# Performance work log

Hardware: AMD Instinct MI355X
Metric: run time of the kernel (lower is better)

## Reference

```python
import jax, jax.numpy as jnp
import numpy as np

D = 1024
H = 16
HD = D // H


def setup_inputs() -> dict:
    key = jax.random.key(0)
    ks = jax.random.split(key, 5)
    s = 1.0 / np.sqrt(D)
    return {
        "inputs": jax.random.normal(ks[0], (2, 2048, D), dtype=jnp.float32),
        "Wq": jax.random.normal(ks[1], (D, D), dtype=jnp.float32) * s,
        "bq": jnp.zeros((D,), jnp.float32),
        "Wk": jax.random.normal(ks[2], (D, D), dtype=jnp.float32) * s,
        "bk": jnp.zeros((D,), jnp.float32),
        "Wv": jax.random.normal(ks[3], (D, D), dtype=jnp.float32) * s,
        "bv": jnp.zeros((D,), jnp.float32),
        "Wo": jax.random.normal(ks[4], (D, D), dtype=jnp.float32) * s,
        "bo": jnp.zeros((D,), jnp.float32),
    }


def reference(inputs, Wq, bq, Wk, bk, Wv, bv, Wo, bo):
    B, S, _ = inputs.shape
    def split_heads(x):  # [B,S,D] -> [B,H,S,hd]
        return x.reshape(B, S, H, HD).transpose(0, 2, 1, 3)
    q = split_heads(inputs @ Wq + bq)
    k = split_heads(inputs @ Wk + bk)
    v = split_heads(inputs @ Wv + bv)
    scale = 1.0 / jnp.sqrt(jnp.asarray(HD, inputs.dtype))
    scores = jnp.einsum("bhsd,bhtd->bhst", q, k) * scale  # [B,H,S,S]
    weights = jax.nn.softmax(scores, axis=-1)
    attn = jnp.einsum("bhst,bhtd->bhsd", weights, v)
    concat = attn.transpose(0, 2, 1, 3).reshape(B, S, D)
    return concat @ Wo + bo
```

## Files before the change

kernel.cpp:

```cpp
#include <hip/hip_runtime.h>


typedef __bf16 bf16x8 __attribute__((ext_vector_type(8)));
typedef float  f32x4  __attribute__((ext_vector_type(4)));

#if __has_builtin(__builtin_amdgcn_exp2f)
#define EXPFN(x) __builtin_amdgcn_exp2f(x)
#define QSCALE (0.125f * 1.44269504088896f)
#else
#define EXPFN(x) __expf(x)
#define QSCALE 0.125f
#endif

#define LDKP 74

__device__ __forceinline__ unsigned short f2bf(float f) {
    unsigned int u = __float_as_uint(f);
    u += 0x7FFFu + ((u >> 16) & 1u);
    return (unsigned short)(u >> 16);
}

__device__ __forceinline__ void gload16(const void* g, void* l) {
    __builtin_amdgcn_global_load_lds(
        (const __attribute__((address_space(1))) void*)g,
        (__attribute__((address_space(3))) void*)l, 16, 0, 0);
}

#define WAIT0_BARRIER() asm volatile("s_waitcnt vmcnt(0)\n\ts_barrier" ::: "memory")

__global__ __launch_bounds__(256) void cast_x_kernel(
    const float4* __restrict__ X, ushort4* __restrict__ Xb, int n4) {
    int i = blockIdx.x * 256 + threadIdx.x;
    if (i < n4) {
        float4 v = X[i];
        ushort4 o;
        o.x = f2bf(v.x); o.y = f2bf(v.y); o.z = f2bf(v.z); o.w = f2bf(v.w);
        Xb[i] = o;
    }
}

__global__ __launch_bounds__(256) void transpose_w_kernel(
    const float* __restrict__ Wq, const float* __restrict__ Wk,
    const float* __restrict__ Wv, const float* __restrict__ Wo,
    unsigned short* __restrict__ Wt_all) {
    __shared__ float tile[32][33];
    const int z = blockIdx.z;
    const float* W = (z == 0) ? Wq : (z == 1) ? Wk : (z == 2) ? Wv : Wo;
    unsigned short* Wt = Wt_all + (size_t)z * 1024 * 1024;
    int c0 = blockIdx.x * 32, r0 = blockIdx.y * 32;
    int x = threadIdx.x, y = threadIdx.y;
    for (int j = 0; j < 32; j += 8)
        tile[y + j][x] = W[(r0 + y + j) * 1024 + c0 + x];
    __syncthreads();
    for (int j = 0; j < 32; j += 8)
        Wt[(c0 + y + j) * 1024 + r0 + x] = f2bf(tile[x][y + j]);
}

__global__ __launch_bounds__(256) void gemm_qkv_kernel(
    const unsigned short* __restrict__ Xb, const unsigned short* __restrict__ Wt_all,
    const float* __restrict__ bq, const float* __restrict__ bk,
    const float* __restrict__ bv,
    unsigned short* __restrict__ Qb, unsigned short* __restrict__ Kb,
    unsigned short* __restrict__ Vt) {
    const int z = blockIdx.z;
    const int x0 = blockIdx.x * 128;
    const int y0 = blockIdx.y * 128;

    const unsigned short* Ap;
    const unsigned short* Bp;
    if (z < 2) {
        Ap = Xb + (size_t)x0 * 1024;
        Bp = Wt_all + (size_t)z * 1024 * 1024 + (size_t)y0 * 1024;
    } else {
        Ap = Wt_all + (size_t)2 * 1024 * 1024 + (size_t)y0 * 1024;
        Bp = Xb + (size_t)x0 * 1024;
    }

    __shared__ __align__(16) unsigned short As[2][128 * 64];
    __shared__ __align__(16) unsigned short Bs[2][128 * 64];

    const int tid = threadIdx.x;
    const int lane = tid & 63, wave = tid >> 6;
    const int quad = lane >> 4, l15 = lane & 15;
    const int wrow = (wave >> 1) * 64, wcol = (wave & 1) * 64;

    f32x4 acc[4][4] = {};

    const int srow = lane >> 3;
    const int ch8  = (lane & 7) * 8;
    const int swz  = (((lane & 7) ^ srow)) * 8;
    const int sw   = (l15 & 7);

    #pragma unroll
    for (int c = 0; c < 4; c++) {
        int r = c * 32 + wave * 8 + srow;
        gload16(Ap + (size_t)r * 1024 + 0 + swz, &As[0][r * 64 + ch8]);
        gload16(Bp + (size_t)r * 1024 + 0 + swz, &Bs[0][r * 64 + ch8]);
    }

    for (int k = 0; k < 16; k++) {
        const int cur = k & 1, nxt = cur ^ 1;
        WAIT0_BARRIER();
        if (k < 15) {
            int k0 = (k + 1) * 64;
            #pragma unroll
            for (int c = 0; c < 4; c++) {
                int r = c * 32 + wave * 8 + srow;
                gload16(Ap + (size_t)r * 1024 + k0 + swz, &As[nxt][r * 64 + ch8]);
                gload16(Bp + (size_t)r * 1024 + k0 + swz, &Bs[nxt][r * 64 + ch8]);
            }
        }
        #pragma unroll
        for (int kk = 0; kk < 2; kk++) {
            bf16x8 af[4], bfr[4];
            #pragma unroll
            for (int i = 0; i < 4; i++)
                af[i] = *(const bf16x8*)&As[cur][(wrow + i * 16 + l15) * 64 +
                                                (((kk * 4 + quad) ^ sw)) * 8];
            #pragma unroll
            for (int j = 0; j < 4; j++)
                bfr[j] = *(const bf16x8*)&Bs[cur][(wcol + j * 16 + l15) * 64 +
                                                 (((kk * 4 + quad) ^ sw)) * 8];
            #pragma unroll
            for (int i = 0; i < 4; i++)
                #pragma unroll
                for (int j = 0; j < 4; j++)
                    acc[i][j] = __builtin_amdgcn_mfma_f32_16x16x32_bf16(
                        af[i], bfr[j], acc[i][j], 0, 0, 0);
        }
    }

    if (z < 2) {
        const float* bias = (z == 0) ? bq : bk;
        #pragma unroll
        for (int j = 0; j < 4; j++) {
            int col = y0 + wcol + j * 16 + l15;
            float bcol = bias[col];
            int h = col >> 6, d = col & 63;
            #pragma unroll
            for (int i = 0; i < 4; i++)
                #pragma unroll
                for (int r = 0; r < 4; r++) {
                    int row = x0 + wrow + i * 16 + quad * 4 + r;
                    int b = row >> 11, s = row & 2047;
                    float v = acc[i][j][r] + bcol;
                    if (z == 0)
                        Qb[(size_t)((b * 16 + h) * 2048 + s) * 64 + d] = f2bf(v * QSCALE);
                    else
                        Kb[(size_t)((b * 16 + h) * 2048 + s) * 64 + d] = f2bf(v);
                }
        }
    } else {
        #pragma unroll
        for (int i = 0; i < 4; i++)
            #pragma unroll
            for (int r = 0; r < 4; r++) {
                int rowd = y0 + wrow + i * 16 + quad * 4 + r;
                float brow = bv[rowd];
                #pragma unroll
                for (int j = 0; j < 4; j++) {
                    int colm = x0 + wcol + j * 16 + l15;
                    int b = colm >> 11, s = colm & 2047;
                    Vt[(size_t)(b * 1024 + rowd) * 2048 + s] = f2bf(acc[i][j][r] + brow);
                }
            }
    }
}

__global__ __launch_bounds__(256) void attn_kernel(
    const unsigned short* __restrict__ Qb, const unsigned short* __restrict__ Kb,
    const unsigned short* __restrict__ Vt, unsigned short* __restrict__ Cc,
    float* __restrict__ Op, float* __restrict__ Lp, int tlen, int do_split) {
    const int bh = blockIdx.y;
    const int b = bh >> 4, h = bh & 15;
    const int q0 = blockIdx.x * 128;
    const int split = blockIdx.z;
    const int tbeg = split * tlen;

    const int tid = threadIdx.x;
    const int lane = tid & 63, wave = tid >> 6;
    const int quad = lane >> 4, l15 = lane & 15;

    __shared__ __align__(16) unsigned short Ks[64 * 64];
    __shared__ __align__(16) unsigned short Vs[64 * 64];
    __shared__ __align__(16) unsigned short Ps[4][32 * LDKP];

    const unsigned short* Qbh = Qb + (size_t)bh * 2048 * 64;
    const unsigned short* Kbh = Kb + (size_t)bh * 2048 * 64;
    const unsigned short* Vbh = Vt + (size_t)bh * 64 * 2048;

    bf16x8 qa[2][2];
    #pragma unroll
    for (int mi = 0; mi < 2; mi++)
        #pragma unroll
        for (int kk = 0; kk < 2; kk++)
            qa[mi][kk] = *(const bf16x8*)&Qbh[
                (size_t)(q0 + wave * 32 + mi * 16 + l15) * 64 + kk * 32 + quad * 8];

    union { unsigned short us[8]; bf16x8 v; } ones_u;
    #pragma unroll
    for (int i = 0; i < 8; i++) ones_u.us[i] = 0x3F80;
    const bf16x8 onesv = ones_u.v;

    f32x4 o[2][4] = {};
    f32x4 ol[2] = {};

    const int srow = lane >> 3;
    const int r0s = wave * 16 + srow;
    const int ch8 = (lane & 7) * 8;
    const int swz = (((lane & 7) ^ srow)) * 8;
    const int sw  = (l15 & 7);

    for (int ti = 0; ti < tlen; ti += 64) {
        const int t0 = tbeg + ti;
        __syncthreads();
        gload16(&Kbh[(size_t)(t0 + r0s) * 64 + swz],       &Ks[r0s * 64 + ch8]);
        gload16(&Kbh[(size_t)(t0 + r0s + 8) * 64 + swz],   &Ks[(r0s + 8) * 64 + ch8]);
        gload16(&Vbh[(size_t)r0s * 2048 + t0 + swz],       &Vs[r0s * 64 + ch8]);
        gload16(&Vbh[(size_t)(r0s + 8) * 2048 + t0 + swz], &Vs[(r0s + 8) * 64 + ch8]);
        asm volatile("s_waitcnt vmcnt(0)" ::: "memory");
        __syncthreads();

        f32x4 sf[2][4] = {};
        #pragma unroll
        for (int j = 0; j < 4; j++)
            #pragma unroll
            for (int kk = 0; kk < 2; kk++) {
                bf16x8 kf = *(const bf16x8*)&Ks[(j * 16 + l15) * 64 +
                                                (((kk * 4 + quad) ^ sw)) * 8];
                sf[0][j] = __builtin_amdgcn_mfma_f32_16x16x32_bf16(qa[0][kk], kf, sf[0][j], 0, 0, 0);
                sf[1][j] = __builtin_amdgcn_mfma_f32_16x16x32_bf16(qa[1][kk], kf, sf[1][j], 0, 0, 0);
            }

        #pragma unroll
        for (int mi = 0; mi < 2; mi++)
            #pragma unroll
            for (int j = 0; j < 4; j++)
                #pragma unroll
                for (int r = 0; r < 4; r++) {
                    float p = EXPFN(sf[mi][j][r]);
                    Ps[wave][(mi * 16 + quad * 4 + r) * LDKP + j * 16 + l15] =
                        (unsigned short)(__float_as_uint(p) >> 16);
                }

        asm volatile("s_waitcnt lgkmcnt(0)" ::: "memory");

        #pragma unroll
        for (int kk = 0; kk < 2; kk++) {
            bf16x8 pf0 = *(const bf16x8*)&Ps[wave][(l15) * LDKP + kk * 32 + quad * 8];
            bf16x8 pf1 = *(const bf16x8*)&Ps[wave][(16 + l15) * LDKP + kk * 32 + quad * 8];
            ol[0] = __builtin_amdgcn_mfma_f32_16x16x32_bf16(pf0, onesv, ol[0], 0, 0, 0);
            ol[1] = __builtin_amdgcn_mfma_f32_16x16x32_bf16(pf1, onesv, ol[1], 0, 0, 0);
            #pragma unroll
            for (int j = 0; j < 4; j++) {
                bf16x8 vf = *(const bf16x8*)&Vs[(j * 16 + l15) * 64 +
                                                (((kk * 4 + quad) ^ sw)) * 8];
                o[0][j] = __builtin_amdgcn_mfma_f32_16x16x32_bf16(pf0, vf, o[0][j], 0, 0, 0);
                o[1][j] = __builtin_amdgcn_mfma_f32_16x16x32_bf16(pf1, vf, o[1][j], 0, 0, 0);
            }
        }
    }

    if (do_split) {
        float* Opd = Op + (size_t)(split * 32 + bh) * 2048 * 64;
        float* Lpd = Lp + (size_t)(split * 32 + bh) * 2048;
        #pragma unroll
        for (int mi = 0; mi < 2; mi++)
            #pragma unroll
            for (int r = 0; r < 4; r++) {
                int s = q0 + wave * 32 + mi * 16 + quad * 4 + r;
                if (l15 == 0) Lpd[s] = ol[mi][r];
                #pragma unroll
                for (int j = 0; j < 4; j++)
                    Opd[(size_t)s * 64 + j * 16 + l15] = o[mi][j][r];
            }
    } else {
        #pragma unroll
        for (int mi = 0; mi < 2; mi++)
            #pragma unroll
            for (int r = 0; r < 4; r++) {
                float inv = 1.f / ol[mi][r];
                int s = q0 + wave * 32 + mi * 16 + quad * 4 + r;
                size_t row = (size_t)(b * 2048 + s);
                #pragma unroll
                for (int j = 0; j < 4; j++)
                    Cc[row * 1024 + h * 64 + j * 16 + l15] = f2bf(o[mi][j][r] * inv);
            }
    }
}

__global__ __launch_bounds__(256) void combine_kernel(
    const float4* __restrict__ Op, const float* __restrict__ Lp,
    unsigned short* __restrict__ Cc) {
    int idx = blockIdx.x * 256 + threadIdx.x;
    int d4 = idx & 15;
    int s = (idx >> 4) & 2047;
    int bh = idx >> 15;
    const size_t half4 = (size_t)32 * 2048 * 16;
    float4 a = Op[(size_t)idx], c = Op[half4 + (size_t)idx];
    float l = Lp[bh * 2048 + s] + Lp[32 * 2048 + bh * 2048 + s];
    float inv = 1.f / l;
    ushort4 o;
    o.x = f2bf((a.x + c.x) * inv); o.y = f2bf((a.y + c.y) * inv);
    o.z = f2bf((a.z + c.z) * inv); o.w = f2bf((a.w + c.w) * inv);
    int b = bh >> 4, h = bh & 15;
    *(ushort4*)&Cc[((size_t)(b * 2048 + s)) * 1024 + h * 64 + d4 * 4] = o;
}

__global__ __launch_bounds__(256) void gemm_out_kernel(
    const unsigned short* __restrict__ Cc, const unsigned short* __restrict__ Wot,
    const float* __restrict__ bo, float* __restrict__ out) {
    const int m0 = blockIdx.x * 128;
    const int n0 = blockIdx.y * 64;

    __shared__ __align__(16) unsigned short As[2][128 * 64];
    __shared__ __align__(16) unsigned short Bs[2][64 * 64];

    const int tid = threadIdx.x;
    const int lane = tid & 63, wave = tid >> 6;
    const int quad = lane >> 4, l15 = lane & 15;
    const int wrow = (wave >> 1) * 64, wcol = (wave & 1) * 32;

    f32x4 acc[4][2] = {};
    const int srow = lane >> 3;
    const int ch8 = (lane & 7) * 8;
    const int swz = (((lane & 7) ^ srow)) * 8;
    const int sw  = (l15 & 7);

    #pragma unroll
    for (int c = 0; c < 4; c++) {
        int r = c * 32 + wave * 8 + srow;
        gload16(Cc + (size_t)(m0 + r) * 1024 + swz, &As[0][r * 64 + ch8]);
        if (c < 2)
            gload16(Wot + (size_t)(n0 + r) * 1024 + swz, &Bs[0][r * 64 + ch8]);
    }

    for (int k = 0; k < 16; k++) {
        const int cur = k & 1, nxt = cur ^ 1;
        WAIT0_BARRIER();
        if (k < 15) {
            int k0 = (k + 1) * 64;
            #pragma unroll
            for (int c = 0; c < 4; c++) {
                int r = c * 32 + wave * 8 + srow;
                gload16(Cc + (size_t)(m0 + r) * 1024 + k0 + swz, &As[nxt][r * 64 + ch8]);
                if (c < 2)
                    gload16(Wot + (size_t)(n0 + r) * 1024 + k0 + swz, &Bs[nxt][r * 64 + ch8]);
            }
        }
        #pragma unroll
        for (int kk = 0; kk < 2; kk++) {
            bf16x8 af[4], bfr[2];
            #pragma unroll
            for (int i = 0; i < 4; i++)
                af[i] = *(const bf16x8*)&As[cur][(wrow + i * 16 + l15) * 64 +
                                                (((kk * 4 + quad) ^ sw)) * 8];
            #pragma unroll
            for (int j = 0; j < 2; j++)
                bfr[j] = *(const bf16x8*)&Bs[cur][(wcol + j * 16 + l15) * 64 +
                                                 (((kk * 4 + quad) ^ sw)) * 8];
            #pragma unroll
            for (int i = 0; i < 4; i++)
                #pragma unroll
                for (int j = 0; j < 2; j++)
                    acc[i][j] = __builtin_amdgcn_mfma_f32_16x16x32_bf16(
                        af[i], bfr[j], acc[i][j], 0, 0, 0);
        }
    }

    #pragma unroll
    for (int j = 0; j < 2; j++) {
        int col = n0 + wcol + j * 16 + l15;
        float bcol = bo[col];
        #pragma unroll
        for (int i = 0; i < 4; i++)
            #pragma unroll
            for (int r = 0; r < 4; r++) {
                int row = m0 + wrow + i * 16 + quad * 4 + r;
                out[(size_t)row * 1024 + col] = acc[i][j][r] + bcol;
            }
    }
}

extern "C" void kernel_launch(void* const* d_in, const int* in_sizes, int n_in,
                              void* d_out, int out_size, void* d_ws, size_t ws_size,
                              hipStream_t stream) {
    const float* X  = (const float*)d_in[0];
    const float* Wq = (const float*)d_in[1];
    const float* bq = (const float*)d_in[2];
    const float* Wk = (const float*)d_in[3];
    const float* bk = (const float*)d_in[4];
    const float* Wv = (const float*)d_in[5];
    const float* bv = (const float*)d_in[6];
    const float* Wo = (const float*)d_in[7];
    const float* bo = (const float*)d_in[8];
    float* out = (float*)d_out;

    char* ws = (char*)d_ws;
    unsigned short* Xb = (unsigned short*)(ws);
    unsigned short* Wt = (unsigned short*)(ws + (8u  << 20));
    unsigned short* Qb = (unsigned short*)(ws + (16u << 20));
    unsigned short* Kb = (unsigned short*)(ws + (24u << 20));
    unsigned short* Vt = (unsigned short*)(ws + (32u << 20));
    unsigned short* Cc = (unsigned short*)(ws + (40u << 20));
    float* Op = (float*)(ws + (48u << 20));
    float* Lp = (float*)(ws + (48u << 20) + 33554432u);
    const bool use_split = ws_size >= ((size_t)(48u << 20) + 33554432u + 524288u);

    cast_x_kernel<<<4096, 256, 0, stream>>>((const float4*)X, (ushort4*)Xb, 1048576);
    transpose_w_kernel<<<dim3(32, 32, 4), dim3(32, 8), 0, stream>>>(Wq, Wk, Wv, Wo, Wt);
    gemm_qkv_kernel<<<dim3(32, 8, 3), 256, 0, stream>>>(Xb, Wt, bq, bk, bv, Qb, Kb, Vt);
    if (use_split) {
        attn_kernel<<<dim3(16, 32, 2), 256, 0, stream>>>(Qb, Kb, Vt, Cc, Op, Lp, 1024, 1);
        combine_kernel<<<4096, 256, 0, stream>>>((const float4*)Op, Lp, Cc);
    } else {
        attn_kernel<<<dim3(16, 32, 1), 256, 0, stream>>>(Qb, Kb, Vt, Cc, Op, Lp, 2048, 0);
    }
    gemm_out_kernel<<<dim3(32, 16), 256, 0, stream>>>(Cc, Wt + 3u * 1024 * 1024, bo, out);
}
```

Baseline: 205.5 us.

## Double-buffer attention K/V tiles, merge prep kernels, widen output GEMM tile

Makes three separate changes. The attention kernel now double-buffers K and V tiles in LDS so the next tile's global-to-LDS load overlaps the current tile's MFMA work. The bf16 cast of X and the weight transposes are merged into one launch. The output projection GEMM tile grows from 128x64 to 128x128, which doubles per-block accumulators and halves the grid. The cost is more LDS and registers per block, which may lower occupancy.

```diff
diff --git a/kernel.cpp b/kernel.cpp
--- a/kernel.cpp
+++ b/kernel.cpp
@@ -28,27 +28,30 @@
 
 #define WAIT0_BARRIER() asm volatile("s_waitcnt vmcnt(0)\n\ts_barrier" ::: "memory")
 
-__global__ __launch_bounds__(256) void cast_x_kernel(
-    const float4* __restrict__ X, ushort4* __restrict__ Xb, int n4) {
-    int i = blockIdx.x * 256 + threadIdx.x;
-    if (i < n4) {
-        float4 v = X[i];
-        ushort4 o;
-        o.x = f2bf(v.x); o.y = f2bf(v.y); o.z = f2bf(v.z); o.w = f2bf(v.w);
-        Xb[i] = o;
-    }
-}
-
-__global__ __launch_bounds__(256) void transpose_w_kernel(
+__global__ __launch_bounds__(256) void prep_kernel(
+    const float* __restrict__ X, ushort4* __restrict__ Xb,
     const float* __restrict__ Wq, const float* __restrict__ Wk,
     const float* __restrict__ Wv, const float* __restrict__ Wo,
     unsigned short* __restrict__ Wt_all) {
+    const int z = blockIdx.z;
+    if (z == 4) {
+        int base = (blockIdx.y * 32 + blockIdx.x) * 1024 + threadIdx.x;
+        const float4* X4 = (const float4*)X;
+        #pragma unroll
+        for (int c = 0; c < 4; c++) {
+            int i = base + c * 256;
+            float4 v = X4[i];
+            ushort4 o;
+            o.x = f2bf(v.x); o.y = f2bf(v.y); o.z = f2bf(v.z); o.w = f2bf(v.w);
+            Xb[i] = o;
+        }
+        return;
+    }
     __shared__ float tile[32][33];
-    const int z = blockIdx.z;
     const float* W = (z == 0) ? Wq : (z == 1) ? Wk : (z == 2) ? Wv : Wo;
     unsigned short* Wt = Wt_all + (size_t)z * 1024 * 1024;
     int c0 = blockIdx.x * 32, r0 = blockIdx.y * 32;
-    int x = threadIdx.x, y = threadIdx.y;
+    int x = threadIdx.x & 31, y = threadIdx.x >> 5;
     for (int j = 0; j < 32; j += 8)
         tile[y + j][x] = W[(r0 + y + j) * 1024 + c0 + x];
     __syncthreads();
@@ -181,8 +184,8 @@
     const int lane = tid & 63, wave = tid >> 6;
     const int quad = lane >> 4, l15 = lane & 15;
 
-    __shared__ __align__(16) unsigned short Ks[64 * 64];
-    __shared__ __align__(16) unsigned short Vs[64 * 64];
+    __shared__ __align__(16) unsigned short Ks[2][64 * 64];
+    __shared__ __align__(16) unsigned short Vs[2][64 * 64];
     __shared__ __align__(16) unsigned short Ps[4][32 * LDKP];
 
     const unsigned short* Qbh = Qb + (size_t)bh * 2048 * 64;
@@ -211,23 +214,33 @@
     const int swz = (((lane & 7) ^ srow)) * 8;
     const int sw  = (l15 & 7);
 
-    for (int ti = 0; ti < tlen; ti += 64) {
-        const int t0 = tbeg + ti;
-        __syncthreads();
-        gload16(&Kbh[(size_t)(t0 + r0s) * 64 + swz],       &Ks[r0s * 64 + ch8]);
-        gload16(&Kbh[(size_t)(t0 + r0s + 8) * 64 + swz],   &Ks[(r0s + 8) * 64 + ch8]);
-        gload16(&Vbh[(size_t)r0s * 2048 + t0 + swz],       &Vs[r0s * 64 + ch8]);
-        gload16(&Vbh[(size_t)(r0s + 8) * 2048 + t0 + swz], &Vs[(r0s + 8) * 64 + ch8]);
-        asm volatile("s_waitcnt vmcnt(0)" ::: "memory");
-        __syncthreads();
+    {
+        const int t0 = tbeg;
+        gload16(&Kbh[(size_t)(t0 + r0s) * 64 + swz],       &Ks[0][r0s * 64 + ch8]);
+        gload16(&Kbh[(size_t)(t0 + r0s + 8) * 64 + swz],   &Ks[0][(r0s + 8) * 64 + ch8]);
+        gload16(&Vbh[(size_t)r0s * 2048 + t0 + swz],       &Vs[0][r0s * 64 + ch8]);
+        gload16(&Vbh[(size_t)(r0s + 8) * 2048 + t0 + swz], &Vs[0][(r0s + 8) * 64 + ch8]);
+    }
+
+    const int niter = tlen >> 6;
+    for (int it = 0; it < niter; it++) {
+        const int cur = it & 1, nxt = cur ^ 1;
+        WAIT0_BARRIER();
+        if (it + 1 < niter) {
+            const int t0 = tbeg + (it + 1) * 64;
+            gload16(&Kbh[(size_t)(t0 + r0s) * 64 + swz],       &Ks[nxt][r0s * 64 + ch8]);
+            gload16(&Kbh[(size_t)(t0 + r0s + 8) * 64 + swz],   &Ks[nxt][(r0s + 8) * 64 + ch8]);
+            gload16(&Vbh[(size_t)r0s * 2048 + t0 + swz],       &Vs[nxt][r0s * 64 + ch8]);
+            gload16(&Vbh[(size_t)(r0s + 8) * 2048 + t0 + swz], &Vs[nxt][(r0s + 8) * 64 + ch8]);
+        }
 
         f32x4 sf[2][4] = {};
         #pragma unroll
         for (int j = 0; j < 4; j++)
             #pragma unroll
             for (int kk = 0; kk < 2; kk++) {
-                bf16x8 kf = *(const bf16x8*)&Ks[(j * 16 + l15) * 64 +
-                                                (((kk * 4 + quad) ^ sw)) * 8];
+                bf16x8 kf = *(const bf16x8*)&Ks[cur][(j * 16 + l15) * 64 +
+                                                     (((kk * 4 + quad) ^ sw)) * 8];
                 sf[0][j] = __builtin_amdgcn_mfma_f32_16x16x32_bf16(qa[0][kk], kf, sf[0][j], 0, 0, 0);
                 sf[1][j] = __builtin_amdgcn_mfma_f32_16x16x32_bf16(qa[1][kk], kf, sf[1][j], 0, 0, 0);
             }
@@ -253,8 +266,8 @@
             ol[1] = __builtin_amdgcn_mfma_f32_16x16x32_bf16(pf1, onesv, ol[1], 0, 0, 0);
             #pragma unroll
             for (int j = 0; j < 4; j++) {
-                bf16x8 vf = *(const bf16x8*)&Vs[(j * 16 + l15) * 64 +
-                                                (((kk * 4 + quad) ^ sw)) * 8];
+                bf16x8 vf = *(const bf16x8*)&Vs[cur][(j * 16 + l15) * 64 +
+                                                     (((kk * 4 + quad) ^ sw)) * 8];
                 o[0][j] = __builtin_amdgcn_mfma_f32_16x16x32_bf16(pf0, vf, o[0][j], 0, 0, 0);
                 o[1][j] = __builtin_amdgcn_mfma_f32_16x16x32_bf16(pf1, vf, o[1][j], 0, 0, 0);
             }
@@ -311,17 +324,17 @@
     const unsigned short* __restrict__ Cc, const unsigned short* __restrict__ Wot,
     const float* __restrict__ bo, float* __restrict__ out) {
     const int m0 = blockIdx.x * 128;
-    const int n0 = blockIdx.y * 64;
+    const int n0 = blockIdx.y * 128;
 
     __shared__ __align__(16) unsigned short As[2][128 * 64];
-    __shared__ __align__(16) unsigned short Bs[2][64 * 64];
+    __shared__ __align__(16) unsigned short Bs[2][128 * 64];
 
     const int tid = threadIdx.x;
     const int lane = tid & 63, wave = tid >> 6;
     const int quad = lane >> 4, l15 = lane & 15;
-    const int wrow = (wave >> 1) * 64, wcol = (wave & 1) * 32;
-
-    f32x4 acc[4][2] = {};
+    const int wrow = (wave >> 1) * 64, wcol = (wave & 1) * 64;
+
+    f32x4 acc[4][4] = {};
     const int srow = lane >> 3;
     const int ch8 = (lane & 7) * 8;
     const int swz = (((lane & 7) ^ srow)) * 8;
@@ -330,9 +343,8 @@
     #pragma unroll
     for (int c = 0; c < 4; c++) {
         int r = c * 32 + wave * 8 + srow;
-        gload16(Cc + (size_t)(m0 + r) * 1024 + swz, &As[0][r * 64 + ch8]);
-        if (c < 2)
-            gload16(Wot + (size_t)(n0 + r) * 1024 + swz, &Bs[0][r * 64 + ch8]);
+        gload16(Cc + (size_t)(m0 + r) * 1024 + swz,  &As[0][r * 64 + ch8]);
+        gload16(Wot + (size_t)(n0 + r) * 1024 + swz, &Bs[0][r * 64 + ch8]);
     }
 
     for (int k = 0; k < 16; k++) {
@@ -343,33 +355,32 @@
             #pragma unroll
             for (int c = 0; c < 4; c++) {
                 int r = c * 32 + wave * 8 + srow;
-                gload16(Cc + (size_t)(m0 + r) * 1024 + k0 + swz, &As[nxt][r * 64 + ch8]);
-                if (c < 2)
-                    gload16(Wot + (size_t)(n0 + r) * 1024 + k0 + swz, &Bs[nxt][r * 64 + ch8]);
+                gload16(Cc + (size_t)(m0 + r) * 1024 + k0 + swz,  &As[nxt][r * 64 + ch8]);
+                gload16(Wot + (size_t)(n0 + r) * 1024 + k0 + swz, &Bs[nxt][r * 64 + ch8]);
             }
         }
         #pragma unroll
         for (int kk = 0; kk < 2; kk++) {
-            bf16x8 af[4], bfr[2];
+            bf16x8 af[4], bfr[4];
             #pragma unroll
             for (int i = 0; i < 4; i++)
                 af[i] = *(const bf16x8*)&As[cur][(wrow + i * 16 + l15) * 64 +
                                                 (((kk * 4 + quad) ^ sw)) * 8];
             #pragma unroll
-            for (int j = 0; j < 2; j++)
+            for (int j = 0; j < 4; j++)
                 bfr[j] = *(const bf16x8*)&Bs[cur][(wcol + j * 16 + l15) * 64 +
                                                  (((kk * 4 + quad) ^ sw)) * 8];
             #pragma unroll
             for (int i = 0; i < 4; i++)
                 #pragma unroll
-                for (int j = 0; j < 2; j++)
+                for (int j = 0; j < 4; j++)
                     acc[i][j] = __builtin_amdgcn_mfma_f32_16x16x32_bf16(
                         af[i], bfr[j], acc[i][j], 0, 0, 0);
         }
     }
 
     #pragma unroll
-    for (int j = 0; j < 2; j++) {
+    for (int j = 0; j < 4; j++) {
         int col = n0 + wcol + j * 16 + l15;
         float bcol = bo[col];
         #pragma unroll
@@ -407,8 +418,7 @@
     float* Lp = (float*)(ws + (48u << 20) + 33554432u);
     const bool use_split = ws_size >= ((size_t)(48u << 20) + 33554432u + 524288u);
 
-    cast_x_kernel<<<4096, 256, 0, stream>>>((const float4*)X, (ushort4*)Xb, 1048576);
-    transpose_w_kernel<<<dim3(32, 32, 4), dim3(32, 8), 0, stream>>>(Wq, Wk, Wv, Wo, Wt);
+    prep_kernel<<<dim3(32, 32, 5), 256, 0, stream>>>(X, (ushort4*)Xb, Wq, Wk, Wv, Wo, Wt);
     gemm_qkv_kernel<<<dim3(32, 8, 3), 256, 0, stream>>>(Xb, Wt, bq, bk, bv, Qb, Kb, Vt);
     if (use_split) {
         attn_kernel<<<dim3(16, 32, 2), 256, 0, stream>>>(Qb, Kb, Vt, Cc, Op, Lp, 1024, 1);
@@ -416,5 +426,5 @@
     } else {
         attn_kernel<<<dim3(16, 32, 1), 256, 0, stream>>>(Qb, Kb, Vt, Cc, Op, Lp, 2048, 0);
     }
-    gemm_out_kernel<<<dim3(32, 16), 256, 0, stream>>>(Cc, Wt + 3u * 1024 * 1024, bo, out);
-}
+    gemm_out_kernel<<<dim3(32, 8), 256, 0, stream>>>(Cc, Wt + 3u * 1024 * 1024, bo, out);
+}
```

New measurement: 217.7 us. 1.06x slower.
